# Optimization experiments

Hardware: AMD Instinct MI355X
Metric: run time of the kernel (lower is better)

## Reference

```python
import jax, jax.numpy as jnp
import numpy as np

D, H, DFF, NE, ND, B = 512, 8, 2048, 64, 64, 16

def _ln(x, g, b):
    m = x.mean(-1, keepdims=True)
    v = ((x - m) ** 2).mean(-1, keepdims=True)
    return (x - m) * jax.lax.rsqrt(v + 1e-5) * g + b

def _mha(q, k, v, Wi, bi, Wo, bo, h=H):
    # q,k,v: (L, B, d) seq-first, like torch nn.MultiheadAttention (eval mode)
    Lq, Bb, d = q.shape
    hd = d // h
    Wq, Wk, Wv = jnp.split(Wi, 3, axis=0)
    bq, bk, bv = jnp.split(bi, 3)
    def proj(x, W, bb):
        y = x @ W.T + bb                                  # (L, B, d)
        return y.reshape(x.shape[0], Bb, h, hd).transpose(1, 2, 0, 3)  # (B, h, L, hd)
    qh = proj(q, Wq, bq) * (hd ** -0.5)
    kh = proj(k, Wk, bk)
    vh = proj(v, Wv, bv)
    a = jax.nn.softmax(jnp.einsum('bhqe,bhke->bhqk', qh, kh), axis=-1)
    o = jnp.einsum('bhqk,bhke->bhqe', a, vh).transpose(2, 0, 1, 3).reshape(Lq, Bb, d)
    return o @ Wo.T + bo

def _ffn(x, W1, b1, W2, b2):
    return jax.nn.relu(x @ W1.T + b1) @ W2.T + b2

def _forward(enc, dec, ec_Wi, ec_bi, ec_Wo, ec_bo, dc_Wi, dc_bi, dc_Wo, dc_bo,
             es_Wi, es_bi, es_Wo, es_bo, ds_Wi, ds_bi, ds_Wo, ds_bo,
             eff_W1, eff_b1, eff_W2, eff_b2, dff_W1, dff_b1, dff_W2, dff_b2,
             n_ec_g, n_ec_b, n_es_g, n_es_b, n_ef_g, n_ef_b, n_dc_g, n_dc_b,
             n_dci_g, n_dci_b, n_ds_g, n_ds_b, n_df_g, n_df_b, pW, pWb, pv, pb):
    f_n = _ln(enc, n_ec_g, n_ec_b)   # (ne, B, d) -- normed once, reused for all j
    G_n = _ln(dec, n_dc_g, n_dc_b)   # (nd, B, d)
    # dec_cross for all j at once (key/value is the single token f_j)
    dc_out = jax.vmap(lambda fj: _mha(G_n, fj[None], fj[None], dc_Wi, dc_bi, dc_Wo, dc_bo))(f_n)  # (ne, nd, B, d)
    G_fj = dec[None] + dc_out                            # (ne, nd, B, d)
    G_im = _ln(G_fj, n_dci_g, n_dci_b)
    # enc_cross for all j at once (query is the single token f_j)
    ec_out = jax.vmap(lambda fj, Gj: _mha(fj[None], Gj, Gj, ec_Wi, ec_bi, ec_Wo, ec_bo)[0])(f_n, G_im)  # (ne, B, d)
    enc1 = enc + ec_out
    # attention pooling over the ne fusion copies
    G_c = G_fj.transpose(2, 1, 0, 3)                     # (B, nd, ne, d)
    energy = jnp.tanh(G_c @ pW.T + pWb + pb)
    w = jax.nn.softmax(energy @ pv.T, axis=2)            # (B, nd, ne, 1)
    dec1 = (G_c * w).sum(axis=2).transpose(1, 0, 2)      # (nd, B, d)
    # self-attention + FFN (pre-norm residual)
    en = _ln(enc1, n_es_g, n_es_b)
    enc2 = enc1 + _mha(en, en, en, es_Wi, es_bi, es_Wo, es_bo)
    dn = _ln(dec1, n_ds_g, n_ds_b)
    dec2 = dec1 + _mha(dn, dn, dn, ds_Wi, ds_bi, ds_Wo, ds_bo)
    enc3 = enc2 + _ffn(_ln(enc2, n_ef_g, n_ef_b), eff_W1, eff_b1, eff_W2, eff_b2)
    dec3 = dec2 + _ffn(_ln(dec2, n_df_g, n_df_b), dff_W1, dff_b1, dff_W2, dff_b2)
    return (enc3, dec3)

def setup_inputs() -> dict:
    key = jax.random.key(0)
    ks = iter(jax.random.split(key, 64))
    def w(shape, scale=0.05):
        return jax.random.normal(next(ks), shape, jnp.float32) * scale
    d, dff = D, DFF
    inp = {
        'enc': jax.random.normal(next(ks), (NE, B, d), jnp.float32),
        'dec': jax.random.normal(next(ks), (ND, B, d), jnp.float32),
    }
    for p in ['ec', 'dc', 'es', 'ds']:
        inp[p + '_Wi'] = w((3 * d, d)); inp[p + '_bi'] = jnp.zeros(3 * d, jnp.float32)
        inp[p + '_Wo'] = w((d, d)); inp[p + '_bo'] = jnp.zeros(d, jnp.float32)
    for p in ['eff', 'dff']:
        inp[p + '_W1'] = w((dff, d)); inp[p + '_b1'] = jnp.zeros(dff, jnp.float32)
        inp[p + '_W2'] = w((d, dff)); inp[p + '_b2'] = jnp.zeros(d, jnp.float32)
    for p in ['n_ec', 'n_es', 'n_ef', 'n_dc', 'n_dci', 'n_ds', 'n_df']:
        inp[p + '_g'] = jnp.ones(d, jnp.float32); inp[p + '_b'] = jnp.zeros(d, jnp.float32)
    inp['pW'] = w((d, d)); inp['pWb'] = jnp.zeros(d, jnp.float32)
    inp['pv'] = w((1, d)); inp['pb'] = jnp.zeros(d, jnp.float32)
    return inp

def reference(enc, dec, ec_Wi, ec_bi, ec_Wo, ec_bo, dc_Wi, dc_bi, dc_Wo, dc_bo,
              es_Wi, es_bi, es_Wo, es_bo, ds_Wi, ds_bi, ds_Wo, ds_bo,
              eff_W1, eff_b1, eff_W2, eff_b2, dff_W1, dff_b1, dff_W2, dff_b2,
              n_ec_g, n_ec_b, n_es_g, n_es_b, n_ef_g, n_ef_b, n_dc_g, n_dc_b,
              n_dci_g, n_dci_b, n_ds_g, n_ds_b, n_df_g, n_df_b, pW, pWb, pv, pb):
    return _forward(enc, dec, ec_Wi, ec_bi, ec_Wo, ec_bo, dc_Wi, dc_bi, dc_Wo, dc_bo,
                    es_Wi, es_bi, es_Wo, es_bo, ds_Wi, ds_bi, ds_Wo, ds_bo,
                    eff_W1, eff_b1, eff_W2, eff_b2, dff_W1, dff_b1, dff_W2, dff_b2,
                    n_ec_g, n_ec_b, n_es_g, n_es_b, n_ef_g, n_ef_b, n_dc_g, n_dc_b,
                    n_dci_g, n_dci_b, n_ds_g, n_ds_b, n_df_g, n_df_b, pW, pWb, pv, pb)
```

## Files before the change

kernel.cpp:

```cpp
#include <hip/hip_runtime.h>


typedef __bf16 bf16_t;
typedef bf16_t bf16x8 __attribute__((ext_vector_type(8)));
typedef float f32x4 __attribute__((ext_vector_type(4)));
typedef unsigned short u16x4 __attribute__((ext_vector_type(4)));
typedef unsigned short u16x8 __attribute__((ext_vector_type(8)));

__device__ inline unsigned short f2bf(float f) {
  unsigned int u = __float_as_uint(f);
  u += 0x7fffu + ((u >> 16) & 1u);
  return (unsigned short)(u >> 16);
}
__device__ inline float bf2f(unsigned short u) {
  return __uint_as_float(((unsigned int)u) << 16);
}

__device__ inline float wsum(float v) {
#pragma unroll
  for (int o = 1; o < 64; o <<= 1) v += __shfl_xor(v, o);
  return v;
}
__device__ inline float wmax(float v) {
#pragma unroll
  for (int o = 1; o < 64; o <<= 1) v = fmaxf(v, __shfl_xor(v, o));
  return v;
}

struct CastJob {
  const float* src;
  unsigned short* dst;
  int n;
  const float* cs;
};

__device__ inline void ln_body(const float* __restrict__ x,
                               const float* __restrict__ g,
                               const float* __restrict__ be,
                               unsigned short* __restrict__ y, int t) {
  float v0 = x[t], v1 = x[t + 256];
  float s = wsum(v0 + v1);
  float s2 = wsum(v0 * v0 + v1 * v1);
  __shared__ float sh[8];
  int w = t >> 6, lane = t & 63;
  if (lane == 0) { sh[w] = s; sh[4 + w] = s2; }
  __syncthreads();
  s = sh[0] + sh[1] + sh[2] + sh[3];
  s2 = sh[4] + sh[5] + sh[6] + sh[7];
  float mean = s * (1.f / 512.f);
  float var = s2 * (1.f / 512.f) - mean * mean;
  float r = rsqrtf(var + 1e-5f);
  y[t] = f2bf((v0 - mean) * r * g[t] + be[t]);
  y[t + 256] = f2bf((v1 - mean) * r * g[t + 256] + be[t + 256]);
}

__device__ inline void stats_body(const float* __restrict__ x,
                                  float* __restrict__ m, float* __restrict__ q2,
                                  unsigned short* __restrict__ xb, int t,
                                  int row) {
  float v0 = x[t], v1 = x[t + 256];
  if (xb) {
    xb[t] = f2bf(v0);
    xb[t + 256] = f2bf(v1);
  }
  float s = wsum(v0 + v1);
  float s2 = wsum(v0 * v0 + v1 * v1);
  __shared__ float sh2[8];
  int w = t >> 6, lane = t & 63;
  if (lane == 0) { sh2[w] = s; sh2[4 + w] = s2; }
  __syncthreads();
  if (t == 0) {
    s = sh2[0] + sh2[1] + sh2[2] + sh2[3];
    s2 = sh2[4] + sh2[5] + sh2[6] + sh2[7];
    m[row] = s * (1.f / 512.f);
    q2[row] = s2 * (1.f / 512.f);
  }
}

struct Phase0Args {
  const float* enc; const float* g_ec; const float* b_ec; unsigned short* f_n;
  const float* dec; float* md; float* q2d; unsigned short* dec_b;
  CastJob cast[6];
  const float* Wk; const float* Wv; const float* bk; const float* bv;
  const float* g_dci; const float* b_dci;
  float* u_k; float* u_v; float* c_k; float* c_v;
  float* zbase; int zcount;
};

__global__ __launch_bounds__(256) void phase0(Phase0Args a) {
  int bx = blockIdx.x;
  const int t = threadIdx.x;
  if (bx < 2048) {
    int row = bx;
    if (row < 1024) {
      ln_body(a.enc + (size_t)row * 512, a.g_ec, a.b_ec,
              a.f_n + (size_t)row * 512, t);
    } else {
      row -= 1024;
      stats_body(a.dec + (size_t)row * 512, a.md, a.q2d,
                 a.dec_b + (size_t)row * 512, t, row);
    }
    return;
  }
  bx -= 2048;
  if (bx < 256) {
    const int total = 6 * 262144;
    const int stride = 256 * 256 * 4;
    for (int e = (bx * 256 + t) * 4; e < total; e += stride) {
      int jj = e >> 18;
      int i = e & 262143;
      const CastJob cj = a.cast[jj];
      float4 v = *(const float4*)(cj.src + i);
      if (cj.cs) {
        int k = i & 511;
        v.x *= cj.cs[k]; v.y *= cj.cs[k + 1];
        v.z *= cj.cs[k + 2]; v.w *= cj.cs[k + 3];
      }
      u16x4 o = {f2bf(v.x), f2bf(v.y), f2bf(v.z), f2bf(v.w)};
      *(u16x4*)(cj.dst + i) = o;
    }
    return;
  }
  bx -= 256;
  if (bx < 128) {
    int n = bx * 4 + (t >> 6);
    int lane = t & 63;
    const float* wk = a.Wk + (size_t)n * 512;
    const float* wv = a.Wv + (size_t)n * 512;
    float uk = 0.f, uv = 0.f, ck = 0.f, cv = 0.f;
#pragma unroll
    for (int k0 = 0; k0 < 512; k0 += 64) {
      int k = k0 + lane;
      float x = wk[k], y = wv[k], gg = a.g_dci[k], bb = a.b_dci[k];
      uk += x * gg; ck += x * bb;
      uv += y * gg; cv += y * bb;
    }
    uk = wsum(uk); uv = wsum(uv); ck = wsum(ck); cv = wsum(cv);
    if (lane == 0) {
      a.u_k[n] = uk; a.u_v[n] = uv;
      a.c_k[n] = ck + a.bk[n]; a.c_v[n] = cv + a.bv[n];
    }
    return;
  }
  for (int i = t; i < a.zcount; i += 256) a.zbase[i] = 0.f;
}

struct GemmJob {
  const unsigned short* X;
  const float* Xf;
  const float* Asum; const float* Asq;
  const float* g; const float* be;
  const unsigned short* W;
  const float* bias;
  const float* resid;
  float* Y;
  unsigned short* Ybf;
  float* Ssum; float* Ssq;
  float scale;
  int relu;
};
struct MrJob {
  const unsigned short* A; const unsigned short* B;
  const float* md; const float* q2d;
  const float* ts; const float* tsq;
  float* mArr; float* rArr;
};
struct GemmBatch {
  GemmJob j[5];
  MrJob mr;
  CastJob c[9];
};

__device__ inline u16x8 fold_pack(float4 va, float4 vb, const float* gp,
                                  const float* bp, float m, float ri) {
  float4 g0 = *(const float4*)gp;
  float4 g1 = *(const float4*)(gp + 4);
  float4 e0 = *(const float4*)bp;
  float4 e1 = *(const float4*)(bp + 4);
  u16x8 o;
  o[0] = f2bf((va.x - m) * ri * g0.x + e0.x);
  o[1] = f2bf((va.y - m) * ri * g0.y + e0.y);
  o[2] = f2bf((va.z - m) * ri * g0.z + e0.z);
  o[3] = f2bf((va.w - m) * ri * g0.w + e0.w);
  o[4] = f2bf((vb.x - m) * ri * g1.x + e1.x);
  o[5] = f2bf((vb.y - m) * ri * g1.y + e1.y);
  o[6] = f2bf((vb.z - m) * ri * g1.z + e1.z);
  o[7] = f2bf((vb.w - m) * ri * g1.w + e1.w);
  return o;
}

__global__ __launch_bounds__(256) void gemm_bf16(GemmBatch gb, int M, int N,
                                                 int K, int cast_z, int mr_z) {
  const int t = threadIdx.x;
  if ((int)blockIdx.z == cast_z) {
    const int nb = gridDim.x * gridDim.y;
    const int bid = blockIdx.y * gridDim.x + blockIdx.x;
    const int stride = nb * 256 * 4;
#pragma unroll 1
    for (int jj = 0; jj < 9; ++jj) {
      const CastJob cj = gb.c[jj];
      if (!cj.src) continue;
      for (int i = (bid * 256 + t) * 4; i < cj.n; i += stride) {
        float4 v = *(const float4*)(cj.src + i);
        u16x4 o = {f2bf(v.x), f2bf(v.y), f2bf(v.z), f2bf(v.w)};
        *(u16x4*)(cj.dst + i) = o;
      }
    }
    return;
  }
  __shared__ unsigned short As[64][72];
  __shared__ unsigned short Bs[64][72];
  const int lane = t & 63;
  const int wave = t >> 6;
  const int wr = wave >> 1;
  const int wc = wave & 1;
  const int fr = lane & 15;
  const int fg = lane >> 4;
  const int c1 = t + 256;
  const int r0 = t >> 3, o0 = (t & 7) * 8;
  const int r1 = c1 >> 3, o1 = (c1 & 7) * 8;

  if ((int)blockIdx.z == mr_z) {
    const int bb = blockIdx.y * gridDim.x + blockIdx.x;
    if (bb >= 16) return;
    const unsigned short* Ap = gb.mr.A + (size_t)bb * 512;
    const unsigned short* Bp = gb.mr.B + (size_t)bb * 512;
    f32x4 acc[2][2] = {};
    for (int k0 = 0; k0 < 512; k0 += 64) {
      *(u16x8*)&As[r0][o0] = *(const u16x8*)&Ap[(size_t)r0 * 8192 + k0 + o0];
      *(u16x8*)&As[r1][o1] = *(const u16x8*)&Ap[(size_t)r1 * 8192 + k0 + o1];
      *(u16x8*)&Bs[r0][o0] = *(const u16x8*)&Bp[(size_t)r0 * 8192 + k0 + o0];
      *(u16x8*)&Bs[r1][o1] = *(const u16x8*)&Bp[(size_t)r1 * 8192 + k0 + o1];
      __syncthreads();
#pragma unroll
      for (int ks = 0; ks < 2; ++ks) {
        int kk = ks * 32 + fg * 8;
        bf16x8 a0 = *(const bf16x8*)&As[wr * 32 + fr][kk];
        bf16x8 a1 = *(const bf16x8*)&As[wr * 32 + 16 + fr][kk];
        bf16x8 b0 = *(const bf16x8*)&Bs[wc * 32 + fr][kk];
        bf16x8 b1 = *(const bf16x8*)&Bs[wc * 32 + 16 + fr][kk];
        acc[0][0] = __builtin_amdgcn_mfma_f32_16x16x32_bf16(a0, b0, acc[0][0], 0, 0, 0);
        acc[0][1] = __builtin_amdgcn_mfma_f32_16x16x32_bf16(a0, b1, acc[0][1], 0, 0, 0);
        acc[1][0] = __builtin_amdgcn_mfma_f32_16x16x32_bf16(a1, b0, acc[1][0], 0, 0, 0);
        acc[1][1] = __builtin_amdgcn_mfma_f32_16x16x32_bf16(a1, b1, acc[1][1], 0, 0, 0);
      }
      __syncthreads();
    }
#pragma unroll
    for (int nt = 0; nt < 2; ++nt) {
      int j = wc * 32 + nt * 16 + fr;
      float mtv = gb.mr.ts[j * 16 + bb] * (1.f / 512.f);
      float qtv = gb.mr.tsq[j * 16 + bb] * (1.f / 512.f);
#pragma unroll
      for (int mt = 0; mt < 2; ++mt) {
        int ibase = wr * 32 + mt * 16 + fg * 4;
#pragma unroll
        for (int r = 0; r < 4; ++r) {
          int i = ibase + r;
          float s = acc[mt][nt][r];
          float mean = gb.mr.md[i * 16 + bb] + mtv;
          float msq = gb.mr.q2d[i * 16 + bb] + qtv + s * (2.f / 512.f);
          int idx = bb * 4096 + j * 64 + i;
          gb.mr.mArr[idx] = mean;
          gb.mr.rArr[idx] = rsqrtf(msq - mean * mean + 1e-5f);
        }
      }
    }
    return;
  }

  const GemmJob jb = gb.j[blockIdx.z];
  const int bm = blockIdx.y * 64;
  const int bn = blockIdx.x * 64;
  const bool fold = jb.Xf != nullptr;
  f32x4 acc[2][2] = {};
  const unsigned short* Wp = jb.W + (size_t)bn * K;
  const unsigned short* Xp = jb.X ? jb.X + (size_t)bm * K : nullptr;

  float lm0 = 0.f, lr0i = 0.f, lm1 = 0.f, lr1i = 0.f;
  if (fold) {
    float s = jb.Asum[bm + r0], q = jb.Asq[bm + r0];
    lm0 = s * (1.f / 512.f);
    lr0i = rsqrtf(q * (1.f / 512.f) - lm0 * lm0 + 1e-5f);
    s = jb.Asum[bm + r1]; q = jb.Asq[bm + r1];
    lm1 = s * (1.f / 512.f);
    lr1i = rsqrtf(q * (1.f / 512.f) - lm1 * lm1 + 1e-5f);
  }

  u16x8 xa0, xa1;
  float4 fa0a, fa0b, fa1a, fa1b;
  if (fold) {
    const float* p0 = jb.Xf + (size_t)(bm + r0) * K + o0;
    const float* p1 = jb.Xf + (size_t)(bm + r1) * K + o1;
    fa0a = *(const float4*)p0; fa0b = *(const float4*)(p0 + 4);
    fa1a = *(const float4*)p1; fa1b = *(const float4*)(p1 + 4);
  } else {
    xa0 = *(const u16x8*)&Xp[(size_t)r0 * K + o0];
    xa1 = *(const u16x8*)&Xp[(size_t)r1 * K + o1];
  }
  u16x8 wa0 = *(const u16x8*)&Wp[(size_t)r0 * K + o0];
  u16x8 wa1 = *(const u16x8*)&Wp[(size_t)r1 * K + o1];

  for (int k0 = 0; k0 < K; k0 += 64) {
    if (fold) {
      *(u16x8*)&As[r0][o0] = fold_pack(fa0a, fa0b, jb.g + k0 + o0, jb.be + k0 + o0, lm0, lr0i);
      *(u16x8*)&As[r1][o1] = fold_pack(fa1a, fa1b, jb.g + k0 + o1, jb.be + k0 + o1, lm1, lr1i);
    } else {
      *(u16x8*)&As[r0][o0] = xa0;
      *(u16x8*)&As[r1][o1] = xa1;
    }
    *(u16x8*)&Bs[r0][o0] = wa0;
    *(u16x8*)&Bs[r1][o1] = wa1;
    __syncthreads();
    if (k0 + 64 < K) {
      const int kn = k0 + 64;
      if (fold) {
        const float* p0 = jb.Xf + (size_t)(bm + r0) * K + kn + o0;
        const float* p1 = jb.Xf + (size_t)(bm + r1) * K + kn + o1;
        fa0a = *(const float4*)p0; fa0b = *(const float4*)(p0 + 4);
        fa1a = *(const float4*)p1; fa1b = *(const float4*)(p1 + 4);
      } else {
        xa0 = *(const u16x8*)&Xp[(size_t)r0 * K + kn + o0];
        xa1 = *(const u16x8*)&Xp[(size_t)r1 * K + kn + o1];
      }
      wa0 = *(const u16x8*)&Wp[(size_t)r0 * K + kn + o0];
      wa1 = *(const u16x8*)&Wp[(size_t)r1 * K + kn + o1];
    }
#pragma unroll
    for (int ks = 0; ks < 2; ++ks) {
      int kk = ks * 32 + fg * 8;
      bf16x8 a0 = *(const bf16x8*)&As[wr * 32 + fr][kk];
      bf16x8 a1 = *(const bf16x8*)&As[wr * 32 + 16 + fr][kk];
      bf16x8 b0 = *(const bf16x8*)&Bs[wc * 32 + fr][kk];
      bf16x8 b1 = *(const bf16x8*)&Bs[wc * 32 + 16 + fr][kk];
      acc[0][0] = __builtin_amdgcn_mfma_f32_16x16x32_bf16(a0, b0, acc[0][0], 0, 0, 0);
      acc[0][1] = __builtin_amdgcn_mfma_f32_16x16x32_bf16(a0, b1, acc[0][1], 0, 0, 0);
      acc[1][0] = __builtin_amdgcn_mfma_f32_16x16x32_bf16(a1, b0, acc[1][0], 0, 0, 0);
      acc[1][1] = __builtin_amdgcn_mfma_f32_16x16x32_bf16(a1, b1, acc[1][1], 0, 0, 0);
    }
    __syncthreads();
  }
  float rsum[2][4], rsq[2][4];
  const bool dostat = jb.Ssum != nullptr;
  if (dostat) {
#pragma unroll
    for (int mt = 0; mt < 2; ++mt)
#pragma unroll
      for (int r = 0; r < 4; ++r) { rsum[mt][r] = 0.f; rsq[mt][r] = 0.f; }
  }
#pragma unroll
  for (int mt = 0; mt < 2; ++mt) {
#pragma unroll
    for (int nt = 0; nt < 2; ++nt) {
      int col = bn + wc * 32 + nt * 16 + fr;
      int rowb = bm + wr * 32 + mt * 16 + fg * 4;
      float bia = jb.bias ? jb.bias[col] : 0.f;
#pragma unroll
      for (int r = 0; r < 4; ++r) {
        float v = (acc[mt][nt][r] + bia) * jb.scale;
        if (jb.relu) v = fmaxf(v, 0.f);
        if (jb.resid) v += jb.resid[(size_t)(rowb + r) * N + col];
        size_t idx = (size_t)(rowb + r) * N + col;
        if (jb.Y) jb.Y[idx] = v;
        if (jb.Ybf) jb.Ybf[idx] = f2bf(v);
        if (dostat) { rsum[mt][r] += v; rsq[mt][r] += v * v; }
      }
    }
  }
  if (dostat) {
#pragma unroll
    for (int mt = 0; mt < 2; ++mt)
#pragma unroll
      for (int r = 0; r < 4; ++r) {
        float s = rsum[mt][r], q = rsq[mt][r];
#pragma unroll
        for (int o = 1; o < 16; o <<= 1) {
          s += __shfl_xor(s, o);
          q += __shfl_xor(q, o);
        }
        if (fr == 0) {
          int row = bm + wr * 32 + mt * 16 + fg * 4 + r;
          atomicAdd(&jb.Ssum[row], s);
          atomicAdd(&jb.Ssq[row], q);
        }
      }
  }
}

__global__ __launch_bounds__(256) void attnpool(
    const unsigned short* __restrict__ Qe, const unsigned short* __restrict__ Kd,
    const unsigned short* __restrict__ Kt, const unsigned short* __restrict__ Vd,
    const unsigned short* __restrict__ Vt, const float* __restrict__ u_k,
    const float* __restrict__ u_v, const float* __restrict__ c_k,
    const float* __restrict__ c_v, const float* __restrict__ mArr,
    const float* __restrict__ rArr, unsigned short* __restrict__ O,
    const float* __restrict__ Ed, const float* __restrict__ Et,
    const float* __restrict__ pv, const float* __restrict__ dec,
    const unsigned short* __restrict__ tbf, float* __restrict__ dec1,
    float* __restrict__ d1s, float* __restrict__ d1q) {
  __shared__ unsigned short Qs[64][72];
  __shared__ unsigned short Ks[64][72];
  __shared__ unsigned short VdT[64][72];
  __shared__ unsigned short Ps[64][72];
  __shared__ float ms[64][66];
  __shared__ float rs[64][66];
  __shared__ float stp[64][4], sup[64][4], scp[64][4];
  __shared__ float stv[64], suv[64], scv[64], swv[64], swmv[64];
  __shared__ float esh[64], wsh[64], pps[8];
  const int t = threadIdx.x;
  if (blockIdx.x < 128) {
    int h = blockIdx.x & 7;
    int b = blockIdx.x >> 3;
    {
      int row = t >> 2;
      int qt = t & 3;
      int cb = qt * 16;
      size_t base = (size_t)(row * 16 + b) * 512 + h * 64 + cb;
      u16x8 q0 = *(const u16x8*)(Qe + base);
      u16x8 q1 = *(const u16x8*)(Qe + base + 8);
      u16x8 k0 = *(const u16x8*)(Kd + base);
      u16x8 k1 = *(const u16x8*)(Kd + base + 8);
      u16x8 kt0 = *(const u16x8*)(Kt + base);
      u16x8 kt1 = *(const u16x8*)(Kt + base + 8);
      u16x8 v0 = *(const u16x8*)(Vd + base);
      u16x8 v1 = *(const u16x8*)(Vd + base + 8);
      *(u16x8*)&Qs[row][cb] = q0;
      *(u16x8*)&Qs[row][cb + 8] = q1;
      *(u16x8*)&Ks[row][cb] = k0;
      *(u16x8*)&Ks[row][cb + 8] = k1;
#pragma unroll
      for (int jj = 0; jj < 8; ++jj) VdT[cb + jj][row] = v0[jj];
#pragma unroll
      for (int jj = 0; jj < 8; ++jj) VdT[cb + 8 + jj][row] = v1[jj];
      float st_ = 0.f, su_ = 0.f, sc_ = 0.f;
#pragma unroll
      for (int jj = 0; jj < 8; ++jj) {
        float qa = bf2f(q0[jj]), qb = bf2f(q1[jj]);
        st_ += qa * bf2f(kt0[jj]) + qb * bf2f(kt1[jj]);
        su_ += qa * u_k[h * 64 + cb + jj] + qb * u_k[h * 64 + cb + 8 + jj];
        sc_ += qa * c_k[h * 64 + cb + jj] + qb * c_k[h * 64 + cb + 8 + jj];
      }
      stp[row][qt] = st_;
      sup[row][qt] = su_;
      scp[row][qt] = sc_;
    }
#pragma unroll
    for (int k = 0; k < 16; ++k) {
      int idx = t + k * 256;
      ms[idx >> 6][idx & 63] = mArr[(size_t)b * 4096 + idx];
      rs[idx >> 6][idx & 63] = rArr[(size_t)b * 4096 + idx];
    }
    __syncthreads();
    if (t < 64) {
      stv[t] = stp[t][0] + stp[t][1] + stp[t][2] + stp[t][3];
      suv[t] = sup[t][0] + sup[t][1] + sup[t][2] + sup[t][3];
      scv[t] = scp[t][0] + scp[t][1] + scp[t][2] + scp[t][3];
    }
    __syncthreads();
    int wave = t >> 6, lane = t & 63;
    int fr = lane & 15, fg = lane >> 4;
    f32x4 sacc[4] = {};
    bf16x8 aq0 = *(const bf16x8*)&Qs[wave * 16 + fr][fg * 8];
    bf16x8 aq1 = *(const bf16x8*)&Qs[wave * 16 + fr][32 + fg * 8];
#pragma unroll
    for (int nt = 0; nt < 4; ++nt) {
      bf16x8 b0 = *(const bf16x8*)&Ks[nt * 16 + fr][fg * 8];
      bf16x8 b1 = *(const bf16x8*)&Ks[nt * 16 + fr][32 + fg * 8];
      sacc[nt] = __builtin_amdgcn_mfma_f32_16x16x32_bf16(aq0, b0, sacc[nt], 0, 0, 0);
      sacc[nt] = __builtin_amdgcn_mfma_f32_16x16x32_bf16(aq1, b1, sacc[nt], 0, 0, 0);
    }
#pragma unroll
    for (int r = 0; r < 4; ++r) {
      int j = wave * 16 + fg * 4 + r;
      float stj = stv[j], suj = suv[j], scj = scv[j];
      float a0, a1, a2, a3;
      {
        int i0 = fr, i1 = 16 + fr, i2 = 32 + fr, i3 = 48 + fr;
        a0 = rs[j][i0] * (sacc[0][r] + stj - ms[j][i0] * suj) + scj;
        a1 = rs[j][i1] * (sacc[1][r] + stj - ms[j][i1] * suj) + scj;
        a2 = rs[j][i2] * (sacc[2][r] + stj - ms[j][i2] * suj) + scj;
        a3 = rs[j][i3] * (sacc[3][r] + stj - ms[j][i3] * suj) + scj;
      }
      float mx = fmaxf(fmaxf(a0, a1), fmaxf(a2, a3));
#pragma unroll
      for (int o = 1; o < 16; o <<= 1) mx = fmaxf(mx, __shfl_xor(mx, o));
      a0 = __expf(a0 - mx);
      a1 = __expf(a1 - mx);
      a2 = __expf(a2 - mx);
      a3 = __expf(a3 - mx);
      float se = a0 + a1 + a2 + a3;
#pragma unroll
      for (int o = 1; o < 16; o <<= 1) se += __shfl_xor(se, o);
      float inv = 1.f / se;
      float w0 = a0 * inv * rs[j][fr];
      float w1 = a1 * inv * rs[j][16 + fr];
      float w2 = a2 * inv * rs[j][32 + fr];
      float w3 = a3 * inv * rs[j][48 + fr];
      float sw = w0 + w1 + w2 + w3;
      float swm = w0 * ms[j][fr] + w1 * ms[j][16 + fr] + w2 * ms[j][32 + fr] +
                  w3 * ms[j][48 + fr];
#pragma unroll
      for (int o = 1; o < 16; o <<= 1) {
        sw += __shfl_xor(sw, o);
        swm += __shfl_xor(swm, o);
      }
      Ps[j][fr] = f2bf(w0);
      Ps[j][16 + fr] = f2bf(w1);
      Ps[j][32 + fr] = f2bf(w2);
      Ps[j][48 + fr] = f2bf(w3);
      if (fr == 0) {
        swv[j] = sw;
        swmv[j] = swm;
      }
    }
    f32x4 oc[4] = {};
    bf16x8 ap0 = *(const bf16x8*)&Ps[wave * 16 + fr][fg * 8];
    bf16x8 ap1 = *(const bf16x8*)&Ps[wave * 16 + fr][32 + fg * 8];
#pragma unroll
    for (int nt = 0; nt < 4; ++nt) {
      bf16x8 b0 = *(const bf16x8*)&VdT[nt * 16 + fr][fg * 8];
      bf16x8 b1 = *(const bf16x8*)&VdT[nt * 16 + fr][32 + fg * 8];
      oc[nt] = __builtin_amdgcn_mfma_f32_16x16x32_bf16(ap0, b0, oc[nt], 0, 0, 0);
      oc[nt] = __builtin_amdgcn_mfma_f32_16x16x32_bf16(ap1, b1, oc[nt], 0, 0, 0);
    }
#pragma unroll
    for (int nt = 0; nt < 4; ++nt) {
      int d = nt * 16 + fr;
      float uvd = u_v[h * 64 + d];
      float cvd = c_v[h * 64 + d];
#pragma unroll
      for (int r = 0; r < 4; ++r) {
        int j = wave * 16 + fg * 4 + r;
        size_t gidx = (size_t)(j * 16 + b) * 512 + h * 64 + d;
        float o = oc[nt][r] + swv[j] * bf2f(Vt[gidx]) - swmv[j] * uvd + cvd;
        O[gidx] = f2bf(o);
      }
    }
    return;
  }
  int idx = blockIdx.x - 128;
  int i = idx & 63;
  int b = idx >> 6;
  int wave = t >> 6, lane = t & 63;
  float edv[8], pvv[8];
  const float* ed = Ed + (size_t)(i * 16 + b) * 512;
#pragma unroll
  for (int c = 0; c < 8; ++c) {
    edv[c] = ed[c * 64 + lane];
    pvv[c] = pv[c * 64 + lane];
  }
#pragma unroll 1
  for (int jl = 0; jl < 16; ++jl) {
    int j = wave * 16 + jl;
    const float* et = Et + (size_t)(j * 16 + b) * 512;
    float s = 0.f;
#pragma unroll
    for (int c = 0; c < 8; ++c) {
      float x = edv[c] + et[c * 64 + lane];
      float e2 = __expf(2.f * x);
      float th = 1.f - 2.f * __builtin_amdgcn_rcpf(e2 + 1.f);
      s += th * pvv[c];
    }
    s = wsum(s);
    if (lane == 0) esh[j] = s;
  }
  __syncthreads();
  if (t < 64) {
    float e = esh[t];
    float mx = wmax(e);
    float ex = __expf(e - mx);
    float se = wsum(ex);
    wsh[t] = ex / se;
  }
  __syncthreads();
  size_t rowib = (size_t)(i * 16 + b) * 512;
  int d2 = t * 2;
  float2 dv = *(const float2*)(dec + rowib + d2);
  float acc0 = dv.x, acc1 = dv.y;
#pragma unroll 8
  for (int j2 = 0; j2 < 64; ++j2) {
    const unsigned short* tp = tbf + (size_t)(j2 * 16 + b) * 512 + d2;
    float w = wsh[j2];
    acc0 += w * bf2f(tp[0]);
    acc1 += w * bf2f(tp[1]);
  }
  float2 ov = {acc0, acc1};
  *(float2*)(dec1 + rowib + d2) = ov;
  float s1 = acc0 + acc1;
  float s2v = acc0 * acc0 + acc1 * acc1;
  s1 = wsum(s1);
  s2v = wsum(s2v);
  if (lane == 0) { pps[wave] = s1; pps[4 + wave] = s2v; }
  __syncthreads();
  if (t == 0) {
    d1s[i * 16 + b] = pps[0] + pps[1] + pps[2] + pps[3];
    d1q[i * 16 + b] = pps[4] + pps[5] + pps[6] + pps[7];
  }
}

__global__ __launch_bounds__(256) void self_attn(
    const unsigned short* __restrict__ QKVe, unsigned short* __restrict__ Oe,
    const unsigned short* __restrict__ QKVd, unsigned short* __restrict__ Od) {
  const unsigned short* QKV = blockIdx.y ? QKVd : QKVe;
  unsigned short* O = blockIdx.y ? Od : Oe;
  int h = blockIdx.x & 7;
  int b = blockIdx.x >> 3;
  __shared__ unsigned short Qs[64][72];
  __shared__ unsigned short Ksh[64][72];
  __shared__ unsigned short VT[64][72];
  __shared__ unsigned short Ps[64][72];
  int t = threadIdx.x;
  {
    int row = t >> 2;
    int cb = (t & 3) * 16;
    const unsigned short* src =
        QKV + (size_t)(row * 16 + b) * 1536 + h * 64 + cb;
    u16x8 q0 = *(const u16x8*)(src);
    u16x8 q1 = *(const u16x8*)(src + 8);
    u16x8 k0 = *(const u16x8*)(src + 512);
    u16x8 k1 = *(const u16x8*)(src + 520);
    u16x8 v0 = *(const u16x8*)(src + 1024);
    u16x8 v1 = *(const u16x8*)(src + 1032);
    *(u16x8*)&Qs[row][cb] = q0;
    *(u16x8*)&Qs[row][cb + 8] = q1;
    *(u16x8*)&Ksh[row][cb] = k0;
    *(u16x8*)&Ksh[row][cb + 8] = k1;
#pragma unroll
    for (int jj = 0; jj < 8; ++jj) VT[cb + jj][row] = v0[jj];
#pragma unroll
    for (int jj = 0; jj < 8; ++jj) VT[cb + 8 + jj][row] = v1[jj];
  }
  __syncthreads();
  int wave = t >> 6, lane = t & 63;
  int fr = lane & 15, fg = lane >> 4;
  f32x4 sc[4] = {};
  bf16x8 aq0 = *(const bf16x8*)&Qs[wave * 16 + fr][fg * 8];
  bf16x8 aq1 = *(const bf16x8*)&Qs[wave * 16 + fr][32 + fg * 8];
#pragma unroll
  for (int nt = 0; nt < 4; ++nt) {
    bf16x8 b0 = *(const bf16x8*)&Ksh[nt * 16 + fr][fg * 8];
    bf16x8 b1 = *(const bf16x8*)&Ksh[nt * 16 + fr][32 + fg * 8];
    sc[nt] = __builtin_amdgcn_mfma_f32_16x16x32_bf16(aq0, b0, sc[nt], 0, 0, 0);
    sc[nt] = __builtin_amdgcn_mfma_f32_16x16x32_bf16(aq1, b1, sc[nt], 0, 0, 0);
  }
#pragma unroll
  for (int r = 0; r < 4; ++r) {
    float a0 = sc[0][r] * 0.125f, a1 = sc[1][r] * 0.125f;
    float a2 = sc[2][r] * 0.125f, a3 = sc[3][r] * 0.125f;
    float mx = fmaxf(fmaxf(a0, a1), fmaxf(a2, a3));
#pragma unroll
    for (int o = 1; o < 16; o <<= 1) mx = fmaxf(mx, __shfl_xor(mx, o));
    a0 = __expf(a0 - mx);
    a1 = __expf(a1 - mx);
    a2 = __expf(a2 - mx);
    a3 = __expf(a3 - mx);
    float se = a0 + a1 + a2 + a3;
#pragma unroll
    for (int o = 1; o < 16; o <<= 1) se += __shfl_xor(se, o);
    float inv = 1.f / se;
    int prow = wave * 16 + fg * 4 + r;
    Ps[prow][0 + fr] = f2bf(a0 * inv);
    Ps[prow][16 + fr] = f2bf(a1 * inv);
    Ps[prow][32 + fr] = f2bf(a2 * inv);
    Ps[prow][48 + fr] = f2bf(a3 * inv);
  }
  f32x4 oc[4] = {};
  bf16x8 ap0 = *(const bf16x8*)&Ps[wave * 16 + fr][fg * 8];
  bf16x8 ap1 = *(const bf16x8*)&Ps[wave * 16 + fr][32 + fg * 8];
#pragma unroll
  for (int nt = 0; nt < 4; ++nt) {
    bf16x8 b0 = *(const bf16x8*)&VT[nt * 16 + fr][fg * 8];
    bf16x8 b1 = *(const bf16x8*)&VT[nt * 16 + fr][32 + fg * 8];
    oc[nt] = __builtin_amdgcn_mfma_f32_16x16x32_bf16(ap0, b0, oc[nt], 0, 0, 0);
    oc[nt] = __builtin_amdgcn_mfma_f32_16x16x32_bf16(ap1, b1, oc[nt], 0, 0, 0);
  }
#pragma unroll
  for (int nt = 0; nt < 4; ++nt) {
#pragma unroll
    for (int r = 0; r < 4; ++r) {
      int q = wave * 16 + fg * 4 + r;
      int d = nt * 16 + fr;
      O[(size_t)(q * 16 + b) * 512 + h * 64 + d] = f2bf(oc[nt][r]);
    }
  }
}

extern "C" void kernel_launch(void* const* d_in, const int* in_sizes, int n_in,
                              void* d_out, int out_size, void* d_ws,
                              size_t ws_size, hipStream_t stream) {
  const float* enc = (const float*)d_in[0];
  const float* dec = (const float*)d_in[1];
  const float* ec_Wi = (const float*)d_in[2];
  const float* ec_bi = (const float*)d_in[3];
  const float* ec_Wo = (const float*)d_in[4];
  const float* ec_bo = (const float*)d_in[5];
  const float* dc_Wi = (const float*)d_in[6];
  const float* dc_bi = (const float*)d_in[7];
  const float* dc_Wo = (const float*)d_in[8];
  const float* dc_bo = (const float*)d_in[9];
  const float* es_Wi = (const float*)d_in[10];
  const float* es_bi = (const float*)d_in[11];
  const float* es_Wo = (const float*)d_in[12];
  const float* es_bo = (const float*)d_in[13];
  const float* ds_Wi = (const float*)d_in[14];
  const float* ds_bi = (const float*)d_in[15];
  const float* ds_Wo = (const float*)d_in[16];
  const float* ds_bo = (const float*)d_in[17];
  const float* eff_W1 = (const float*)d_in[18];
  const float* eff_b1 = (const float*)d_in[19];
  const float* eff_W2 = (const float*)d_in[20];
  const float* eff_b2 = (const float*)d_in[21];
  const float* dff_W1 = (const float*)d_in[22];
  const float* dff_b1 = (const float*)d_in[23];
  const float* dff_W2 = (const float*)d_in[24];
  const float* dff_b2 = (const float*)d_in[25];
  const float* n_ec_g = (const float*)d_in[26];
  const float* n_ec_b = (const float*)d_in[27];
  const float* n_es_g = (const float*)d_in[28];
  const float* n_es_b = (const float*)d_in[29];
  const float* n_ef_g = (const float*)d_in[30];
  const float* n_ef_b = (const float*)d_in[31];
  const float* n_dci_g = (const float*)d_in[34];
  const float* n_dci_b = (const float*)d_in[35];
  const float* n_ds_g = (const float*)d_in[36];
  const float* n_ds_b = (const float*)d_in[37];
  const float* n_df_g = (const float*)d_in[38];
  const float* n_df_b = (const float*)d_in[39];
  const float* pW = (const float*)d_in[40];
  const float* pWb = (const float*)d_in[41];
  const float* pv = (const float*)d_in[42];
  const float* pb = (const float*)d_in[43];

  float* ws = (float*)d_ws;
  const size_t U = 524288;
  float* Ed = ws + 3 * U;
  float* Et = ws + 7 * U;
  float* enc1 = ws + 8 * U;
  float* dec1 = ws + 9 * U;
  float* enc2 = ws + 10 * U;
  float* dec2 = ws + 11 * U;
  float* sm = ws + 12 * U;
  float* md = sm;
  float* q2d = sm + 1024;
  float* u_k = sm + 4096;
  float* u_v = sm + 4608;
  float* c_k = sm + 5120;
  float* c_v = sm + 5632;
  float* mArr = sm + 6144;
  float* rArr = sm + 6144 + 65536;
  float* stx = ws + 24 * U;
  float* t_s = stx;
  float* t_sq = stx + 1024;
  float* e1s = stx + 2048;
  float* e1q = stx + 3072;
  float* d1s = stx + 4096;
  float* d1q = stx + 5120;
  float* e2s = stx + 6144;
  float* e2q = stx + 7168;
  float* d2s = stx + 8192;
  float* d2q = stx + 9216;
  unsigned short* ub0 = (unsigned short*)ws;
  unsigned short* Qe_b = ub0 + 0 * U;
  unsigned short* Kd_b = ub0 + 1 * U;
  unsigned short* Vd_b = ub0 + 2 * U;
  unsigned short* Kt_b = ub0 + 3 * U;
  unsigned short* Vt_b = ub0 + 4 * U;
  unsigned short* ub = (unsigned short*)(ws + 12 * U + 137216);
  const int W262 = 262144, W786 = 786432, W1M = 1048576;
  unsigned short* w_dcWv = ub;
  unsigned short* w_ecWq = w_dcWv + W262;
  unsigned short* w_ecWkg = w_ecWq + W262;
  unsigned short* w_ecWvg = w_ecWkg + W262;
  unsigned short* w_pW = w_ecWvg + W262;
  unsigned short* w_dcWo = w_pW + W262;
  unsigned short* w_ecWo = w_dcWo + W262;
  unsigned short* w_esWi = w_ecWo + W262;
  unsigned short* w_dsWi = w_esWi + W786;
  unsigned short* w_esWo = w_dsWi + W786;
  unsigned short* w_dsWo = w_esWo + W262;
  unsigned short* w_effW1 = w_dsWo + W262;
  unsigned short* w_dffW1 = w_effW1 + W1M;
  unsigned short* w_effW2 = w_dffW1 + W1M;
  unsigned short* w_dffW2 = w_effW2 + W1M;
  unsigned short* actb = w_dffW2 + W1M;
  unsigned short* f_n_b = actb;
  unsigned short* V1_b = actb + U;
  unsigned short* dec_b = actb + 2 * U;
  unsigned short* tb_b = actb + 3 * U;
  unsigned short* Oec_b = actb + 4 * U;
  unsigned short* OaE = dec_b;
  unsigned short* OaD = tb_b;
  unsigned short* QKVe_b = (unsigned short*)(ws + 0 * U);
  unsigned short* QKVd_b = (unsigned short*)(ws + 2 * U);
  unsigned short* He_b = (unsigned short*)(ws + 0 * U);
  unsigned short* Hd_b = (unsigned short*)(ws + 2 * U);

  const float* dc_Wv = dc_Wi + 1024 * 512;
  const float* dc_bv = dc_bi + 1024;
  const float* ec_Wq = ec_Wi;
  const float* ec_bq = ec_bi;
  const float* ec_Wk = ec_Wi + 512 * 512;
  const float* ec_bk = ec_bi + 512;
  const float* ec_Wv = ec_Wi + 1024 * 512;
  const float* ec_bv = ec_bi + 1024;

  auto J = [](const unsigned short* X, const unsigned short* W,
              const float* bias, const float* resid, float* Y,
              unsigned short* Ybf, float scale, int relu) {
    GemmJob j{};
    j.X = X; j.W = W; j.bias = bias; j.resid = resid;
    j.Y = Y; j.Ybf = Ybf; j.scale = scale; j.relu = relu;
    return j;
  };
  auto JF = [](const float* Xf, const float* As, const float* Aq,
               const float* g, const float* be, const unsigned short* W,
               const float* bias, unsigned short* Ybf, int relu) {
    GemmJob j{};
    j.Xf = Xf; j.Asum = As; j.Asq = Aq; j.g = g; j.be = be;
    j.W = W; j.bias = bias; j.Ybf = Ybf; j.scale = 1.f; j.relu = relu;
    return j;
  };

  {
    Phase0Args pa{};
    pa.enc = enc; pa.g_ec = n_ec_g; pa.b_ec = n_ec_b; pa.f_n = f_n_b;
    pa.dec = dec; pa.md = md; pa.q2d = q2d; pa.dec_b = dec_b;
    pa.cast[0] = {dc_Wv, w_dcWv, W262, nullptr};
    pa.cast[1] = {ec_Wq, w_ecWq, W262, nullptr};
    pa.cast[2] = {ec_Wk, w_ecWkg, W262, n_dci_g};
    pa.cast[3] = {ec_Wv, w_ecWvg, W262, n_dci_g};
    pa.cast[4] = {pW, w_pW, W262, nullptr};
    pa.cast[5] = {dc_Wo, w_dcWo, W262, nullptr};
    pa.Wk = ec_Wk; pa.Wv = ec_Wv; pa.bk = ec_bk; pa.bv = ec_bv;
    pa.g_dci = n_dci_g; pa.b_dci = n_dci_b;
    pa.u_k = u_k; pa.u_v = u_v; pa.c_k = c_k; pa.c_v = c_v;
    pa.zbase = stx; pa.zcount = 10240;
    phase0<<<2433, 256, 0, stream>>>(pa);
  }
  {
    GemmBatch gb{};
    gb.j[0] = J(f_n_b, w_dcWv, dc_bv, nullptr, nullptr, V1_b, 1.f, 0);
    gb.j[1] = J(f_n_b, w_ecWq, ec_bq, nullptr, nullptr, Qe_b, 0.125f, 0);
    gb.j[2] = J(dec_b, w_ecWkg, nullptr, nullptr, nullptr, Kd_b, 1.f, 0);
    gb.j[3] = J(dec_b, w_ecWvg, nullptr, nullptr, nullptr, Vd_b, 1.f, 0);
    gb.j[4] = J(dec_b, w_pW, pWb, nullptr, Ed, nullptr, 1.f, 0);
    gb.c[0] = {ec_Wo, w_ecWo, W262, nullptr};
    gb.c[1] = {es_Wi, w_esWi, W786, nullptr};
    gb.c[2] = {ds_Wi, w_dsWi, W786, nullptr};
    gb.c[3] = {es_Wo, w_esWo, W262, nullptr};
    gb.c[4] = {ds_Wo, w_dsWo, W262, nullptr};
    gb.c[5] = {eff_W1, w_effW1, W1M, nullptr};
    gb.c[6] = {dff_W1, w_dffW1, W1M, nullptr};
    gb.c[7] = {eff_W2, w_effW2, W1M, nullptr};
    gb.c[8] = {dff_W2, w_dffW2, W1M, nullptr};
    gemm_bf16<<<dim3(8, 16, 6), 256, 0, stream>>>(gb, 1024, 512, 512, 5, -1);
  }
  {
    GemmBatch gb{};
    gb.j[0] = J(V1_b, w_dcWo, dc_bo, nullptr, nullptr, tb_b, 1.f, 0);
    gb.j[0].Ssum = t_s; gb.j[0].Ssq = t_sq;
    gemm_bf16<<<dim3(8, 16, 1), 256, 0, stream>>>(gb, 1024, 512, 512, -1, -1);
  }
  {
    GemmBatch gb{};
    gb.j[0] = J(tb_b, w_ecWkg, nullptr, nullptr, nullptr, Kt_b, 1.f, 0);
    gb.j[1] = J(tb_b, w_ecWvg, nullptr, nullptr, nullptr, Vt_b, 1.f, 0);
    gb.j[2] = J(tb_b, w_pW, pb, nullptr, Et, nullptr, 1.f, 0);
    gb.mr = {dec_b, tb_b, md, q2d, t_s, t_sq, mArr, rArr};
    gemm_bf16<<<dim3(8, 16, 4), 256, 0, stream>>>(gb, 1024, 512, 512, -1, 3);
  }
  attnpool<<<1152, 256, 0, stream>>>(Qe_b, Kd_b, Kt_b, Vd_b, Vt_b, u_k, u_v,
                                     c_k, c_v, mArr, rArr, Oec_b, Ed, Et, pv,
                                     dec, tb_b, dec1, d1s, d1q);
  {
    GemmBatch gb{};
    gb.j[0] = J(Oec_b, w_ecWo, ec_bo, enc, enc1, nullptr, 1.f, 0);
    gb.j[0].Ssum = e1s; gb.j[0].Ssq = e1q;
    gemm_bf16<<<dim3(8, 16, 1), 256, 0, stream>>>(gb, 1024, 512, 512, -1, -1);
  }
  {
    GemmBatch gb{};
    gb.j[0] = JF(enc1, e1s, e1q, n_es_g, n_es_b, w_esWi, es_bi, QKVe_b, 0);
    gb.j[1] = JF(dec1, d1s, d1q, n_ds_g, n_ds_b, w_dsWi, ds_bi, QKVd_b, 0);
    gemm_bf16<<<dim3(24, 16, 2), 256, 0, stream>>>(gb, 1024, 1536, 512, -1, -1);
  }
  self_attn<<<dim3(128, 2), 256, 0, stream>>>(QKVe_b, OaE, QKVd_b, OaD);
  {
    GemmBatch gb{};
    gb.j[0] = J(OaE, w_esWo, es_bo, enc1, enc2, nullptr, 1.f, 0);
    gb.j[0].Ssum = e2s; gb.j[0].Ssq = e2q;
    gb.j[1] = J(OaD, w_dsWo, ds_bo, dec1, dec2, nullptr, 1.f, 0);
    gb.j[1].Ssum = d2s; gb.j[1].Ssq = d2q;
    gemm_bf16<<<dim3(8, 16, 2), 256, 0, stream>>>(gb, 1024, 512, 512, -1, -1);
  }
  {
    GemmBatch gb{};
    gb.j[0] = JF(enc2, e2s, e2q, n_ef_g, n_ef_b, w_effW1, eff_b1, He_b, 1);
    gb.j[1] = JF(dec2, d2s, d2q, n_df_g, n_df_b, w_dffW1, dff_b1, Hd_b, 1);
    gemm_bf16<<<dim3(32, 16, 2), 256, 0, stream>>>(gb, 1024, 2048, 512, -1, -1);
  }
  float* out = (float*)d_out;
  {
    GemmBatch gb{};
    gb.j[0] = J(He_b, w_effW2, eff_b2, enc2, out, nullptr, 1.f, 0);
    gb.j[1] = J(Hd_b, w_dffW2, dff_b2, dec2, out + U, nullptr, 1.f, 0);
    gemm_bf16<<<dim3(8, 16, 2), 256, 0, stream>>>(gb, 1024, 512, 2048, -1, -1);
  }
}
```

Baseline: 339.8 us.

## Move attention pooling into ec_Wo GEMM launch and template GEMM variants

The attention-pooling work moves out of the combined attnpool kernel and into extra z-slices of the following ec_Wo GEMM launch, so ec_attn now runs alone with 128 blocks and pooling overlaps the GEMM. The GEMM kernel is templated on its extra-work mode, LayerNorm folding and stats epilogue, which turns runtime branches into compile-time ones. Pooling now competes with the GEMM for the same launch and shares its LDS footprint, which may lower occupancy for the pooling blocks.

```diff
diff --git a/kernel.cpp b/kernel.cpp
--- a/kernel.cpp
+++ b/kernel.cpp
@@ -165,10 +165,15 @@
   const float* ts; const float* tsq;
   float* mArr; float* rArr;
 };
+struct PoolJob {
+  const float* Ed; const float* Et; const float* pv; const float* dec;
+  const unsigned short* tbf; float* dec1; float* d1s; float* d1q;
+};
 struct GemmBatch {
   GemmJob j[5];
   MrJob mr;
   CastJob c[9];
+  PoolJob pl;
 };
 
 __device__ inline u16x8 fold_pack(float4 va, float4 vb, const float* gp,
@@ -189,24 +194,95 @@
   return o;
 }
 
+__device__ void pool_body(const PoolJob& p, int i, int b) {
+  __shared__ float esh[64], wsh[64], pps[8];
+  const int t = threadIdx.x;
+  int wave = t >> 6, lane = t & 63;
+  float edv[8], pvv[8];
+  const float* ed = p.Ed + (size_t)(i * 16 + b) * 512;
+#pragma unroll
+  for (int c = 0; c < 8; ++c) {
+    edv[c] = ed[c * 64 + lane];
+    pvv[c] = p.pv[c * 64 + lane];
+  }
+#pragma unroll 1
+  for (int jl = 0; jl < 16; ++jl) {
+    int j = wave * 16 + jl;
+    const float* et = p.Et + (size_t)(j * 16 + b) * 512;
+    float s = 0.f;
+#pragma unroll
+    for (int c = 0; c < 8; ++c) {
+      float x = edv[c] + et[c * 64 + lane];
+      float e2 = __expf(2.f * x);
+      float th = 1.f - 2.f * __builtin_amdgcn_rcpf(e2 + 1.f);
+      s += th * pvv[c];
+    }
+    s = wsum(s);
+    if (lane == 0) esh[j] = s;
+  }
+  __syncthreads();
+  if (t < 64) {
+    float e = esh[t];
+    float mx = wmax(e);
+    float ex = __expf(e - mx);
+    float se = wsum(ex);
+    wsh[t] = ex / se;
+  }
+  __syncthreads();
+  size_t rowib = (size_t)(i * 16 + b) * 512;
+  int d2 = t * 2;
+  float2 dv = *(const float2*)(p.dec + rowib + d2);
+  float acc0 = dv.x, acc1 = dv.y;
+#pragma unroll 8
+  for (int j2 = 0; j2 < 64; ++j2) {
+    const unsigned short* tp = p.tbf + (size_t)(j2 * 16 + b) * 512 + d2;
+    float w = wsh[j2];
+    acc0 += w * bf2f(tp[0]);
+    acc1 += w * bf2f(tp[1]);
+  }
+  float2 ov = {acc0, acc1};
+  *(float2*)(p.dec1 + rowib + d2) = ov;
+  float s1 = acc0 + acc1;
+  float s2v = acc0 * acc0 + acc1 * acc1;
+  s1 = wsum(s1);
+  s2v = wsum(s2v);
+  if (lane == 0) { pps[wave] = s1; pps[4 + wave] = s2v; }
+  __syncthreads();
+  if (t == 0) {
+    p.d1s[i * 16 + b] = pps[0] + pps[1] + pps[2] + pps[3];
+    p.d1q[i * 16 + b] = pps[4] + pps[5] + pps[6] + pps[7];
+  }
+}
+
+template <int EXTRA, bool FOLD, bool STATS>
 __global__ __launch_bounds__(256) void gemm_bf16(GemmBatch gb, int M, int N,
-                                                 int K, int cast_z, int mr_z) {
+                                                 int K, int xz) {
   const int t = threadIdx.x;
-  if ((int)blockIdx.z == cast_z) {
-    const int nb = gridDim.x * gridDim.y;
-    const int bid = blockIdx.y * gridDim.x + blockIdx.x;
-    const int stride = nb * 256 * 4;
+  if constexpr (EXTRA == 1) {
+    if ((int)blockIdx.z == xz) {
+      const int nb = gridDim.x * gridDim.y;
+      const int bid = blockIdx.y * gridDim.x + blockIdx.x;
+      const int stride = nb * 256 * 4;
 #pragma unroll 1
-    for (int jj = 0; jj < 9; ++jj) {
-      const CastJob cj = gb.c[jj];
-      if (!cj.src) continue;
-      for (int i = (bid * 256 + t) * 4; i < cj.n; i += stride) {
-        float4 v = *(const float4*)(cj.src + i);
-        u16x4 o = {f2bf(v.x), f2bf(v.y), f2bf(v.z), f2bf(v.w)};
-        *(u16x4*)(cj.dst + i) = o;
+      for (int jj = 0; jj < 9; ++jj) {
+        const CastJob cj = gb.c[jj];
+        if (!cj.src) continue;
+        for (int i = (bid * 256 + t) * 4; i < cj.n; i += stride) {
+          float4 v = *(const float4*)(cj.src + i);
+          u16x4 o = {f2bf(v.x), f2bf(v.y), f2bf(v.z), f2bf(v.w)};
+          *(u16x4*)(cj.dst + i) = o;
+        }
       }
-    }
-    return;
+      return;
+    }
+  }
+  if constexpr (EXTRA == 3) {
+    if ((int)blockIdx.z >= xz) {
+      int pb = ((int)blockIdx.z - xz) * (int)(gridDim.x * gridDim.y) +
+               (int)blockIdx.y * (int)gridDim.x + (int)blockIdx.x;
+      pool_body(gb.pl, pb & 63, pb >> 6);
+      return;
+    }
   }
   __shared__ unsigned short As[64][72];
   __shared__ unsigned short Bs[64][72];
@@ -220,81 +296,80 @@
   const int r0 = t >> 3, o0 = (t & 7) * 8;
   const int r1 = c1 >> 3, o1 = (c1 & 7) * 8;
 
-  if ((int)blockIdx.z == mr_z) {
-    const int bb = blockIdx.y * gridDim.x + blockIdx.x;
-    if (bb >= 16) return;
-    const unsigned short* Ap = gb.mr.A + (size_t)bb * 512;
-    const unsigned short* Bp = gb.mr.B + (size_t)bb * 512;
-    f32x4 acc[2][2] = {};
-    for (int k0 = 0; k0 < 512; k0 += 64) {
-      *(u16x8*)&As[r0][o0] = *(const u16x8*)&Ap[(size_t)r0 * 8192 + k0 + o0];
-      *(u16x8*)&As[r1][o1] = *(const u16x8*)&Ap[(size_t)r1 * 8192 + k0 + o1];
-      *(u16x8*)&Bs[r0][o0] = *(const u16x8*)&Bp[(size_t)r0 * 8192 + k0 + o0];
-      *(u16x8*)&Bs[r1][o1] = *(const u16x8*)&Bp[(size_t)r1 * 8192 + k0 + o1];
-      __syncthreads();
-#pragma unroll
-      for (int ks = 0; ks < 2; ++ks) {
-        int kk = ks * 32 + fg * 8;
-        bf16x8 a0 = *(const bf16x8*)&As[wr * 32 + fr][kk];
-        bf16x8 a1 = *(const bf16x8*)&As[wr * 32 + 16 + fr][kk];
-        bf16x8 b0 = *(const bf16x8*)&Bs[wc * 32 + fr][kk];
-        bf16x8 b1 = *(const bf16x8*)&Bs[wc * 32 + 16 + fr][kk];
-        acc[0][0] = __builtin_amdgcn_mfma_f32_16x16x32_bf16(a0, b0, acc[0][0], 0, 0, 0);
-        acc[0][1] = __builtin_amdgcn_mfma_f32_16x16x32_bf16(a0, b1, acc[0][1], 0, 0, 0);
-        acc[1][0] = __builtin_amdgcn_mfma_f32_16x16x32_bf16(a1, b0, acc[1][0], 0, 0, 0);
-        acc[1][1] = __builtin_amdgcn_mfma_f32_16x16x32_bf16(a1, b1, acc[1][1], 0, 0, 0);
+  if constexpr (EXTRA == 2) {
+    if ((int)blockIdx.z == xz) {
+      const int bb = blockIdx.y * gridDim.x + blockIdx.x;
+      if (bb >= 16) return;
+      const unsigned short* Ap = gb.mr.A + (size_t)bb * 512;
+      const unsigned short* Bp = gb.mr.B + (size_t)bb * 512;
+      f32x4 acc[2][2] = {};
+      for (int k0 = 0; k0 < 512; k0 += 64) {
+        *(u16x8*)&As[r0][o0] = *(const u16x8*)&Ap[(size_t)r0 * 8192 + k0 + o0];
+        *(u16x8*)&As[r1][o1] = *(const u16x8*)&Ap[(size_t)r1 * 8192 + k0 + o1];
+        *(u16x8*)&Bs[r0][o0] = *(const u16x8*)&Bp[(size_t)r0 * 8192 + k0 + o0];
+        *(u16x8*)&Bs[r1][o1] = *(const u16x8*)&Bp[(size_t)r1 * 8192 + k0 + o1];
+        __syncthreads();
+#pragma unroll
+        for (int ks = 0; ks < 2; ++ks) {
+          int kk = ks * 32 + fg * 8;
+          bf16x8 a0 = *(const bf16x8*)&As[wr * 32 + fr][kk];
+          bf16x8 a1 = *(const bf16x8*)&As[wr * 32 + 16 + fr][kk];
+          bf16x8 b0 = *(const bf16x8*)&Bs[wc * 32 + fr][kk];
+          bf16x8 b1 = *(const bf16x8*)&Bs[wc * 32 + 16 + fr][kk];
+          acc[0][0] = __builtin_amdgcn_mfma_f32_16x16x32_bf16(a0, b0, acc[0][0], 0, 0, 0);
+          acc[0][1] = __builtin_amdgcn_mfma_f32_16x16x32_bf16(a0, b1, acc[0][1], 0, 0, 0);
+          acc[1][0] = __builtin_amdgcn_mfma_f32_16x16x32_bf16(a1, b0, acc[1][0], 0, 0, 0);
+          acc[1][1] = __builtin_amdgcn_mfma_f32_16x16x32_bf16(a1, b1, acc[1][1], 0, 0, 0);
+        }
+        __syncthreads();
       }
-      __syncthreads();
-    }
-#pragma unroll
-    for (int nt = 0; nt < 2; ++nt) {
-      int j = wc * 32 + nt * 16 + fr;
-      float mtv = gb.mr.ts[j * 16 + bb] * (1.f / 512.f);
-      float qtv = gb.mr.tsq[j * 16 + bb] * (1.f / 512.f);
-#pragma unroll
-      for (int mt = 0; mt < 2; ++mt) {
-        int ibase = wr * 32 + mt * 16 + fg * 4;
-#pragma unroll
-        for (int r = 0; r < 4; ++r) {
-          int i = ibase + r;
-          float s = acc[mt][nt][r];
-          float mean = gb.mr.md[i * 16 + bb] + mtv;
-          float msq = gb.mr.q2d[i * 16 + bb] + qtv + s * (2.f / 512.f);
-          int idx = bb * 4096 + j * 64 + i;
-          gb.mr.mArr[idx] = mean;
-          gb.mr.rArr[idx] = rsqrtf(msq - mean * mean + 1e-5f);
+#pragma unroll
+      for (int nt = 0; nt < 2; ++nt) {
+        int j = wc * 32 + nt * 16 + fr;
+        float mtv = gb.mr.ts[j * 16 + bb] * (1.f / 512.f);
+        float qtv = gb.mr.tsq[j * 16 + bb] * (1.f / 512.f);
+#pragma unroll
+        for (int mt = 0; mt < 2; ++mt) {
+          int ibase = wr * 32 + mt * 16 + fg * 4;
+#pragma unroll
+          for (int r = 0; r < 4; ++r) {
+            int i = ibase + r;
+            float s = acc[mt][nt][r];
+            float mean = gb.mr.md[i * 16 + bb] + mtv;
+            float msq = gb.mr.q2d[i * 16 + bb] + qtv + s * (2.f / 512.f);
+            int idx = bb * 4096 + j * 64 + i;
+            gb.mr.mArr[idx] = mean;
+            gb.mr.rArr[idx] = rsqrtf(msq - mean * mean + 1e-5f);
+          }
         }
       }
-    }
-    return;
+      return;
+    }
   }
 
   const GemmJob jb = gb.j[blockIdx.z];
   const int bm = blockIdx.y * 64;
   const int bn = blockIdx.x * 64;
-  const bool fold = jb.Xf != nullptr;
   f32x4 acc[2][2] = {};
   const unsigned short* Wp = jb.W + (size_t)bn * K;
-  const unsigned short* Xp = jb.X ? jb.X + (size_t)bm * K : nullptr;
-
+
+  u16x8 xa0, xa1;
+  float4 fa0a, fa0b, fa1a, fa1b;
   float lm0 = 0.f, lr0i = 0.f, lm1 = 0.f, lr1i = 0.f;
-  if (fold) {
+  const unsigned short* Xp = nullptr;
+  if constexpr (FOLD) {
     float s = jb.Asum[bm + r0], q = jb.Asq[bm + r0];
     lm0 = s * (1.f / 512.f);
     lr0i = rsqrtf(q * (1.f / 512.f) - lm0 * lm0 + 1e-5f);
     s = jb.Asum[bm + r1]; q = jb.Asq[bm + r1];
     lm1 = s * (1.f / 512.f);
     lr1i = rsqrtf(q * (1.f / 512.f) - lm1 * lm1 + 1e-5f);
-  }
-
-  u16x8 xa0, xa1;
-  float4 fa0a, fa0b, fa1a, fa1b;
-  if (fold) {
     const float* p0 = jb.Xf + (size_t)(bm + r0) * K + o0;
     const float* p1 = jb.Xf + (size_t)(bm + r1) * K + o1;
     fa0a = *(const float4*)p0; fa0b = *(const float4*)(p0 + 4);
     fa1a = *(const float4*)p1; fa1b = *(const float4*)(p1 + 4);
   } else {
+    Xp = jb.X + (size_t)bm * K;
     xa0 = *(const u16x8*)&Xp[(size_t)r0 * K + o0];
     xa1 = *(const u16x8*)&Xp[(size_t)r1 * K + o1];
   }
@@ -302,7 +377,7 @@
   u16x8 wa1 = *(const u16x8*)&Wp[(size_t)r1 * K + o1];
 
   for (int k0 = 0; k0 < K; k0 += 64) {
-    if (fold) {
+    if constexpr (FOLD) {
       *(u16x8*)&As[r0][o0] = fold_pack(fa0a, fa0b, jb.g + k0 + o0, jb.be + k0 + o0, lm0, lr0i);
       *(u16x8*)&As[r1][o1] = fold_pack(fa1a, fa1b, jb.g + k0 + o1, jb.be + k0 + o1, lm1, lr1i);
     } else {
@@ -314,7 +389,7 @@
     __syncthreads();
     if (k0 + 64 < K) {
       const int kn = k0 + 64;
-      if (fold) {
+      if constexpr (FOLD) {
         const float* p0 = jb.Xf + (size_t)(bm + r0) * K + kn + o0;
         const float* p1 = jb.Xf + (size_t)(bm + r1) * K + kn + o1;
         fa0a = *(const float4*)p0; fa0b = *(const float4*)(p0 + 4);
@@ -341,8 +416,7 @@
     __syncthreads();
   }
   float rsum[2][4], rsq[2][4];
-  const bool dostat = jb.Ssum != nullptr;
-  if (dostat) {
+  if constexpr (STATS) {
 #pragma unroll
     for (int mt = 0; mt < 2; ++mt)
 #pragma unroll
@@ -363,11 +437,11 @@
         size_t idx = (size_t)(rowb + r) * N + col;
         if (jb.Y) jb.Y[idx] = v;
         if (jb.Ybf) jb.Ybf[idx] = f2bf(v);
-        if (dostat) { rsum[mt][r] += v; rsq[mt][r] += v * v; }
+        if constexpr (STATS) { rsum[mt][r] += v; rsq[mt][r] += v * v; }
       }
     }
   }
-  if (dostat) {
+  if constexpr (STATS) {
 #pragma unroll
     for (int mt = 0; mt < 2; ++mt)
 #pragma unroll
@@ -387,17 +461,15 @@
   }
 }
 
-__global__ __launch_bounds__(256) void attnpool(
+__global__ __launch_bounds__(256) void ec_attn(
     const unsigned short* __restrict__ Qe, const unsigned short* __restrict__ Kd,
     const unsigned short* __restrict__ Kt, const unsigned short* __restrict__ Vd,
     const unsigned short* __restrict__ Vt, const float* __restrict__ u_k,
     const float* __restrict__ u_v, const float* __restrict__ c_k,
     const float* __restrict__ c_v, const float* __restrict__ mArr,
-    const float* __restrict__ rArr, unsigned short* __restrict__ O,
-    const float* __restrict__ Ed, const float* __restrict__ Et,
-    const float* __restrict__ pv, const float* __restrict__ dec,
-    const unsigned short* __restrict__ tbf, float* __restrict__ dec1,
-    float* __restrict__ d1s, float* __restrict__ d1q) {
+    const float* __restrict__ rArr, unsigned short* __restrict__ O) {
+  int h = blockIdx.x & 7;
+  int b = blockIdx.x >> 3;
   __shared__ unsigned short Qs[64][72];
   __shared__ unsigned short Ks[64][72];
   __shared__ unsigned short VdT[64][72];
@@ -406,195 +478,131 @@
   __shared__ float rs[64][66];
   __shared__ float stp[64][4], sup[64][4], scp[64][4];
   __shared__ float stv[64], suv[64], scv[64], swv[64], swmv[64];
-  __shared__ float esh[64], wsh[64], pps[8];
-  const int t = threadIdx.x;
-  if (blockIdx.x < 128) {
-    int h = blockIdx.x & 7;
-    int b = blockIdx.x >> 3;
+  int t = threadIdx.x;
+  {
+    int row = t >> 2;
+    int qt = t & 3;
+    int cb = qt * 16;
+    size_t base = (size_t)(row * 16 + b) * 512 + h * 64 + cb;
+    u16x8 q0 = *(const u16x8*)(Qe + base);
+    u16x8 q1 = *(const u16x8*)(Qe + base + 8);
+    u16x8 k0 = *(const u16x8*)(Kd + base);
+    u16x8 k1 = *(const u16x8*)(Kd + base + 8);
+    u16x8 kt0 = *(const u16x8*)(Kt + base);
+    u16x8 kt1 = *(const u16x8*)(Kt + base + 8);
+    u16x8 v0 = *(const u16x8*)(Vd + base);
+    u16x8 v1 = *(const u16x8*)(Vd + base + 8);
+    *(u16x8*)&Qs[row][cb] = q0;
+    *(u16x8*)&Qs[row][cb + 8] = q1;
+    *(u16x8*)&Ks[row][cb] = k0;
+    *(u16x8*)&Ks[row][cb + 8] = k1;
+#pragma unroll
+    for (int jj = 0; jj < 8; ++jj) VdT[cb + jj][row] = v0[jj];
+#pragma unroll
+    for (int jj = 0; jj < 8; ++jj) VdT[cb + 8 + jj][row] = v1[jj];
+    float st_ = 0.f, su_ = 0.f, sc_ = 0.f;
+#pragma unroll
+    for (int jj = 0; jj < 8; ++jj) {
+      float qa = bf2f(q0[jj]), qb = bf2f(q1[jj]);
+      st_ += qa * bf2f(kt0[jj]) + qb * bf2f(kt1[jj]);
+      su_ += qa * u_k[h * 64 + cb + jj] + qb * u_k[h * 64 + cb + 8 + jj];
+      sc_ += qa * c_k[h * 64 + cb + jj] + qb * c_k[h * 64 + cb + 8 + jj];
+    }
+    stp[row][qt] = st_;
+    sup[row][qt] = su_;
+    scp[row][qt] = sc_;
+  }
+#pragma unroll
+  for (int k = 0; k < 16; ++k) {
+    int idx = t + k * 256;
+    ms[idx >> 6][idx & 63] = mArr[(size_t)b * 4096 + idx];
+    rs[idx >> 6][idx & 63] = rArr[(size_t)b * 4096 + idx];
+  }
+  __syncthreads();
+  if (t < 64) {
+    stv[t] = stp[t][0] + stp[t][1] + stp[t][2] + stp[t][3];
+    suv[t] = sup[t][0] + sup[t][1] + sup[t][2] + sup[t][3];
+    scv[t] = scp[t][0] + scp[t][1] + scp[t][2] + scp[t][3];
+  }
+  __syncthreads();
+  int wave = t >> 6, lane = t & 63;
+  int fr = lane & 15, fg = lane >> 4;
+  f32x4 sacc[4] = {};
+  bf16x8 aq0 = *(const bf16x8*)&Qs[wave * 16 + fr][fg * 8];
+  bf16x8 aq1 = *(const bf16x8*)&Qs[wave * 16 + fr][32 + fg * 8];
+#pragma unroll
+  for (int nt = 0; nt < 4; ++nt) {
+    bf16x8 b0 = *(const bf16x8*)&Ks[nt * 16 + fr][fg * 8];
+    bf16x8 b1 = *(const bf16x8*)&Ks[nt * 16 + fr][32 + fg * 8];
+    sacc[nt] = __builtin_amdgcn_mfma_f32_16x16x32_bf16(aq0, b0, sacc[nt], 0, 0, 0);
+    sacc[nt] = __builtin_amdgcn_mfma_f32_16x16x32_bf16(aq1, b1, sacc[nt], 0, 0, 0);
+  }
+#pragma unroll
+  for (int r = 0; r < 4; ++r) {
+    int j = wave * 16 + fg * 4 + r;
+    float stj = stv[j], suj = suv[j], scj = scv[j];
+    float a0, a1, a2, a3;
     {
-      int row = t >> 2;
-      int qt = t & 3;
-      int cb = qt * 16;
-      size_t base = (size_t)(row * 16 + b) * 512 + h * 64 + cb;
-      u16x8 q0 = *(const u16x8*)(Qe + base);
-      u16x8 q1 = *(const u16x8*)(Qe + base + 8);
-      u16x8 k0 = *(const u16x8*)(Kd + base);
-      u16x8 k1 = *(const u16x8*)(Kd + base + 8);
-      u16x8 kt0 = *(const u16x8*)(Kt + base);
-      u16x8 kt1 = *(const u16x8*)(Kt + base + 8);
-      u16x8 v0 = *(const u16x8*)(Vd + base);
-      u16x8 v1 = *(const u16x8*)(Vd + base + 8);
-      *(u16x8*)&Qs[row][cb] = q0;
-      *(u16x8*)&Qs[row][cb + 8] = q1;
-      *(u16x8*)&Ks[row][cb] = k0;
-      *(u16x8*)&Ks[row][cb + 8] = k1;
-#pragma unroll
-      for (int jj = 0; jj < 8; ++jj) VdT[cb + jj][row] = v0[jj];
-#pragma unroll
-      for (int jj = 0; jj < 8; ++jj) VdT[cb + 8 + jj][row] = v1[jj];
-      float st_ = 0.f, su_ = 0.f, sc_ = 0.f;
-#pragma unroll
-      for (int jj = 0; jj < 8; ++jj) {
-        float qa = bf2f(q0[jj]), qb = bf2f(q1[jj]);
-        st_ += qa * bf2f(kt0[jj]) + qb * bf2f(kt1[jj]);
-        su_ += qa * u_k[h * 64 + cb + jj] + qb * u_k[h * 64 + cb + 8 + jj];
-        sc_ += qa * c_k[h * 64 + cb + jj] + qb * c_k[h * 64 + cb + 8 + jj];
-      }
-      stp[row][qt] = st_;
-      sup[row][qt] = su_;
-      scp[row][qt] = sc_;
-    }
-#pragma unroll
-    for (int k = 0; k < 16; ++k) {
-      int idx = t + k * 256;
-      ms[idx >> 6][idx & 63] = mArr[(size_t)b * 4096 + idx];
-      rs[idx >> 6][idx & 63] = rArr[(size_t)b * 4096 + idx];
-    }
-    __syncthreads();
-    if (t < 64) {
-      stv[t] = stp[t][0] + stp[t][1] + stp[t][2] + stp[t][3];
-      suv[t] = sup[t][0] + sup[t][1] + sup[t][2] + sup[t][3];
-      scv[t] = scp[t][0] + scp[t][1] + scp[t][2] + scp[t][3];
-    }
-    __syncthreads();
-    int wave = t >> 6, lane = t & 63;
-    int fr = lane & 15, fg = lane >> 4;
-    f32x4 sacc[4] = {};
-    bf16x8 aq0 = *(const bf16x8*)&Qs[wave * 16 + fr][fg * 8];
-    bf16x8 aq1 = *(const bf16x8*)&Qs[wave * 16 + fr][32 + fg * 8];
-#pragma unroll
-    for (int nt = 0; nt < 4; ++nt) {
-      bf16x8 b0 = *(const bf16x8*)&Ks[nt * 16 + fr][fg * 8];
-      bf16x8 b1 = *(const bf16x8*)&Ks[nt * 16 + fr][32 + fg * 8];
-      sacc[nt] = __builtin_amdgcn_mfma_f32_16x16x32_bf16(aq0, b0, sacc[nt], 0, 0, 0);
-      sacc[nt] = __builtin_amdgcn_mfma_f32_16x16x32_bf16(aq1, b1, sacc[nt], 0, 0, 0);
-    }
+      int i0 = fr, i1 = 16 + fr, i2 = 32 + fr, i3 = 48 + fr;
+      a0 = rs[j][i0] * (sacc[0][r] + stj - ms[j][i0] * suj) + scj;
+      a1 = rs[j][i1] * (sacc[1][r] + stj - ms[j][i1] * suj) + scj;
+      a2 = rs[j][i2] * (sacc[2][r] + stj - ms[j][i2] * suj) + scj;
+      a3 = rs[j][i3] * (sacc[3][r] + stj - ms[j][i3] * suj) + scj;
+    }
+    float mx = fmaxf(fmaxf(a0, a1), fmaxf(a2, a3));
+#pragma unroll
+    for (int o = 1; o < 16; o <<= 1) mx = fmaxf(mx, __shfl_xor(mx, o));
+    a0 = __expf(a0 - mx);
+    a1 = __expf(a1 - mx);
+    a2 = __expf(a2 - mx);
+    a3 = __expf(a3 - mx);
+    float se = a0 + a1 + a2 + a3;
+#pragma unroll
+    for (int o = 1; o < 16; o <<= 1) se += __shfl_xor(se, o);
+    float inv = 1.f / se;
+    float w0 = a0 * inv * rs[j][fr];
+    float w1 = a1 * inv * rs[j][16 + fr];
+    float w2 = a2 * inv * rs[j][32 + fr];
+    float w3 = a3 * inv * rs[j][48 + fr];
+    float sw = w0 + w1 + w2 + w3;
+    float swm = w0 * ms[j][fr] + w1 * ms[j][16 + fr] + w2 * ms[j][32 + fr] +
+                w3 * ms[j][48 + fr];
+#pragma unroll
+    for (int o = 1; o < 16; o <<= 1) {
+      sw += __shfl_xor(sw, o);
+      swm += __shfl_xor(swm, o);
+    }
+    Ps[j][fr] = f2bf(w0);
+    Ps[j][16 + fr] = f2bf(w1);
+    Ps[j][32 + fr] = f2bf(w2);
+    Ps[j][48 + fr] = f2bf(w3);
+    if (fr == 0) {
+      swv[j] = sw;
+      swmv[j] = swm;
+    }
+  }
+  f32x4 oc[4] = {};
+  bf16x8 ap0 = *(const bf16x8*)&Ps[wave * 16 + fr][fg * 8];
+  bf16x8 ap1 = *(const bf16x8*)&Ps[wave * 16 + fr][32 + fg * 8];
+#pragma unroll
+  for (int nt = 0; nt < 4; ++nt) {
+    bf16x8 b0 = *(const bf16x8*)&VdT[nt * 16 + fr][fg * 8];
+    bf16x8 b1 = *(const bf16x8*)&VdT[nt * 16 + fr][32 + fg * 8];
+    oc[nt] = __builtin_amdgcn_mfma_f32_16x16x32_bf16(ap0, b0, oc[nt], 0, 0, 0);
+    oc[nt] = __builtin_amdgcn_mfma_f32_16x16x32_bf16(ap1, b1, oc[nt], 0, 0, 0);
+  }
+#pragma unroll
+  for (int nt = 0; nt < 4; ++nt) {
+    int d = nt * 16 + fr;
+    float uvd = u_v[h * 64 + d];
+    float cvd = c_v[h * 64 + d];
 #pragma unroll
     for (int r = 0; r < 4; ++r) {
       int j = wave * 16 + fg * 4 + r;
-      float stj = stv[j], suj = suv[j], scj = scv[j];
-      float a0, a1, a2, a3;
-      {
-        int i0 = fr, i1 = 16 + fr, i2 = 32 + fr, i3 = 48 + fr;
-        a0 = rs[j][i0] * (sacc[0][r] + stj - ms[j][i0] * suj) + scj;
-        a1 = rs[j][i1] * (sacc[1][r] + stj - ms[j][i1] * suj) + scj;
-        a2 = rs[j][i2] * (sacc[2][r] + stj - ms[j][i2] * suj) + scj;
-        a3 = rs[j][i3] * (sacc[3][r] + stj - ms[j][i3] * suj) + scj;
-      }
-      float mx = fmaxf(fmaxf(a0, a1), fmaxf(a2, a3));
-#pragma unroll
-      for (int o = 1; o < 16; o <<= 1) mx = fmaxf(mx, __shfl_xor(mx, o));
-      a0 = __expf(a0 - mx);
-      a1 = __expf(a1 - mx);
-      a2 = __expf(a2 - mx);
-      a3 = __expf(a3 - mx);
-      float se = a0 + a1 + a2 + a3;
-#pragma unroll
-      for (int o = 1; o < 16; o <<= 1) se += __shfl_xor(se, o);
-      float inv = 1.f / se;
-      float w0 = a0 * inv * rs[j][fr];
-      float w1 = a1 * inv * rs[j][16 + fr];
-      float w2 = a2 * inv * rs[j][32 + fr];
-      float w3 = a3 * inv * rs[j][48 + fr];
-      float sw = w0 + w1 + w2 + w3;
-      float swm = w0 * ms[j][fr] + w1 * ms[j][16 + fr] + w2 * ms[j][32 + fr] +
-                  w3 * ms[j][48 + fr];
-#pragma unroll
-      for (int o = 1; o < 16; o <<= 1) {
-        sw += __shfl_xor(sw, o);
-        swm += __shfl_xor(swm, o);
-      }
-      Ps[j][fr] = f2bf(w0);
-      Ps[j][16 + fr] = f2bf(w1);
-      Ps[j][32 + fr] = f2bf(w2);
-      Ps[j][48 + fr] = f2bf(w3);
-      if (fr == 0) {
-        swv[j] = sw;
-        swmv[j] = swm;
-      }
-    }
-    f32x4 oc[4] = {};
-    bf16x8 ap0 = *(const bf16x8*)&Ps[wave * 16 + fr][fg * 8];
-    bf16x8 ap1 = *(const bf16x8*)&Ps[wave * 16 + fr][32 + fg * 8];
-#pragma unroll
-    for (int nt = 0; nt < 4; ++nt) {
-      bf16x8 b0 = *(const bf16x8*)&VdT[nt * 16 + fr][fg * 8];
-      bf16x8 b1 = *(const bf16x8*)&VdT[nt * 16 + fr][32 + fg * 8];
-      oc[nt] = __builtin_amdgcn_mfma_f32_16x16x32_bf16(ap0, b0, oc[nt], 0, 0, 0);
-      oc[nt] = __builtin_amdgcn_mfma_f32_16x16x32_bf16(ap1, b1, oc[nt], 0, 0, 0);
-    }
-#pragma unroll
-    for (int nt = 0; nt < 4; ++nt) {
-      int d = nt * 16 + fr;
-      float uvd = u_v[h * 64 + d];
-      float cvd = c_v[h * 64 + d];
-#pragma unroll
-      for (int r = 0; r < 4; ++r) {
-        int j = wave * 16 + fg * 4 + r;
-        size_t gidx = (size_t)(j * 16 + b) * 512 + h * 64 + d;
-        float o = oc[nt][r] + swv[j] * bf2f(Vt[gidx]) - swmv[j] * uvd + cvd;
-        O[gidx] = f2bf(o);
-      }
-    }
-    return;
-  }
-  int idx = blockIdx.x - 128;
-  int i = idx & 63;
-  int b = idx >> 6;
-  int wave = t >> 6, lane = t & 63;
-  float edv[8], pvv[8];
-  const float* ed = Ed + (size_t)(i * 16 + b) * 512;
-#pragma unroll
-  for (int c = 0; c < 8; ++c) {
-    edv[c] = ed[c * 64 + lane];
-    pvv[c] = pv[c * 64 + lane];
-  }
-#pragma unroll 1
-  for (int jl = 0; jl < 16; ++jl) {
-    int j = wave * 16 + jl;
-    const float* et = Et + (size_t)(j * 16 + b) * 512;
-    float s = 0.f;
-#pragma unroll
-    for (int c = 0; c < 8; ++c) {
-      float x = edv[c] + et[c * 64 + lane];
-      float e2 = __expf(2.f * x);
-      float th = 1.f - 2.f * __builtin_amdgcn_rcpf(e2 + 1.f);
-      s += th * pvv[c];
-    }
-    s = wsum(s);
-    if (lane == 0) esh[j] = s;
-  }
-  __syncthreads();
-  if (t < 64) {
-    float e = esh[t];
-    float mx = wmax(e);
-    float ex = __expf(e - mx);
-    float se = wsum(ex);
-    wsh[t] = ex / se;
-  }
-  __syncthreads();
-  size_t rowib = (size_t)(i * 16 + b) * 512;
-  int d2 = t * 2;
-  float2 dv = *(const float2*)(dec + rowib + d2);
-  float acc0 = dv.x, acc1 = dv.y;
-#pragma unroll 8
-  for (int j2 = 0; j2 < 64; ++j2) {
-    const unsigned short* tp = tbf + (size_t)(j2 * 16 + b) * 512 + d2;
-    float w = wsh[j2];
-    acc0 += w * bf2f(tp[0]);
-    acc1 += w * bf2f(tp[1]);
-  }
-  float2 ov = {acc0, acc1};
-  *(float2*)(dec1 + rowib + d2) = ov;
-  float s1 = acc0 + acc1;
-  float s2v = acc0 * acc0 + acc1 * acc1;
-  s1 = wsum(s1);
-  s2v = wsum(s2v);
-  if (lane == 0) { pps[wave] = s1; pps[4 + wave] = s2v; }
-  __syncthreads();
-  if (t == 0) {
-    d1s[i * 16 + b] = pps[0] + pps[1] + pps[2] + pps[3];
-    d1q[i * 16 + b] = pps[4] + pps[5] + pps[6] + pps[7];
+      size_t gidx = (size_t)(j * 16 + b) * 512 + h * 64 + d;
+      float o = oc[nt][r] + swv[j] * bf2f(Vt[gidx]) - swmv[j] * uvd + cvd;
+      O[gidx] = f2bf(o);
+    }
   }
 }
 
@@ -853,13 +861,15 @@
     gb.c[6] = {dff_W1, w_dffW1, W1M, nullptr};
     gb.c[7] = {eff_W2, w_effW2, W1M, nullptr};
     gb.c[8] = {dff_W2, w_dffW2, W1M, nullptr};
-    gemm_bf16<<<dim3(8, 16, 6), 256, 0, stream>>>(gb, 1024, 512, 512, 5, -1);
+    gemm_bf16<1, false, false><<<dim3(8, 16, 6), 256, 0, stream>>>(
+        gb, 1024, 512, 512, 5);
   }
   {
     GemmBatch gb{};
     gb.j[0] = J(V1_b, w_dcWo, dc_bo, nullptr, nullptr, tb_b, 1.f, 0);
     gb.j[0].Ssum = t_s; gb.j[0].Ssq = t_sq;
-    gemm_bf16<<<dim3(8, 16, 1), 256, 0, stream>>>(gb, 1024, 512, 512, -1, -1);
+    gemm_bf16<0, false, true><<<dim3(8, 16, 1), 256, 0, stream>>>(
+        gb, 1024, 512, 512, -1);
   }
   {
     GemmBatch gb{};
@@ -867,22 +877,25 @@
     gb.j[1] = J(tb_b, w_ecWvg, nullptr, nullptr, nullptr, Vt_b, 1.f, 0);
     gb.j[2] = J(tb_b, w_pW, pb, nullptr, Et, nullptr, 1.f, 0);
     gb.mr = {dec_b, tb_b, md, q2d, t_s, t_sq, mArr, rArr};
-    gemm_bf16<<<dim3(8, 16, 4), 256, 0, stream>>>(gb, 1024, 512, 512, -1, 3);
-  }
-  attnpool<<<1152, 256, 0, stream>>>(Qe_b, Kd_b, Kt_b, Vd_b, Vt_b, u_k, u_v,
-                                     c_k, c_v, mArr, rArr, Oec_b, Ed, Et, pv,
-                                     dec, tb_b, dec1, d1s, d1q);
+    gemm_bf16<2, false, false><<<dim3(8, 16, 4), 256, 0, stream>>>(
+        gb, 1024, 512, 512, 3);
+  }
+  ec_attn<<<128, 256, 0, stream>>>(Qe_b, Kd_b, Kt_b, Vd_b, Vt_b, u_k, u_v, c_k,
+                                   c_v, mArr, rArr, Oec_b);
   {
     GemmBatch gb{};
     gb.j[0] = J(Oec_b, w_ecWo, ec_bo, enc, enc1, nullptr, 1.f, 0);
     gb.j[0].Ssum = e1s; gb.j[0].Ssq = e1q;
-    gemm_bf16<<<dim3(8, 16, 1), 256, 0, stream>>>(gb, 1024, 512, 512, -1, -1);
+    gb.pl = {Ed, Et, pv, dec, tb_b, dec1, d1s, d1q};
+    gemm_bf16<3, false, true><<<dim3(8, 16, 9), 256, 0, stream>>>(
+        gb, 1024, 512, 512, 1);
   }
   {
     GemmBatch gb{};
     gb.j[0] = JF(enc1, e1s, e1q, n_es_g, n_es_b, w_esWi, es_bi, QKVe_b, 0);
     gb.j[1] = JF(dec1, d1s, d1q, n_ds_g, n_ds_b, w_dsWi, ds_bi, QKVd_b, 0);
-    gemm_bf16<<<dim3(24, 16, 2), 256, 0, stream>>>(gb, 1024, 1536, 512, -1, -1);
+    gemm_bf16<0, true, false><<<dim3(24, 16, 2), 256, 0, stream>>>(
+        gb, 1024, 1536, 512, -1);
   }
   self_attn<<<dim3(128, 2), 256, 0, stream>>>(QKVe_b, OaE, QKVd_b, OaD);
   {
@@ -891,19 +904,22 @@
     gb.j[0].Ssum = e2s; gb.j[0].Ssq = e2q;
     gb.j[1] = J(OaD, w_dsWo, ds_bo, dec1, dec2, nullptr, 1.f, 0);
     gb.j[1].Ssum = d2s; gb.j[1].Ssq = d2q;
-    gemm_bf16<<<dim3(8, 16, 2), 256, 0, stream>>>(gb, 1024, 512, 512, -1, -1);
+    gemm_bf16<0, false, true><<<dim3(8, 16, 2), 256, 0, stream>>>(
+        gb, 1024, 512, 512, -1);
   }
   {
     GemmBatch gb{};
     gb.j[0] = JF(enc2, e2s, e2q, n_ef_g, n_ef_b, w_effW1, eff_b1, He_b, 1);
     gb.j[1] = JF(dec2, d2s, d2q, n_df_g, n_df_b, w_dffW1, dff_b1, Hd_b, 1);
-    gemm_bf16<<<dim3(32, 16, 2), 256, 0, stream>>>(gb, 1024, 2048, 512, -1, -1);
+    gemm_bf16<0, true, false><<<dim3(32, 16, 2), 256, 0, stream>>>(
+        gb, 1024, 2048, 512, -1);
   }
   float* out = (float*)d_out;
   {
     GemmBatch gb{};
     gb.j[0] = J(He_b, w_effW2, eff_b2, enc2, out, nullptr, 1.f, 0);
     gb.j[1] = J(Hd_b, w_dffW2, dff_b2, dec2, out + U, nullptr, 1.f, 0);
-    gemm_bf16<<<dim3(8, 16, 2), 256, 0, stream>>>(gb, 1024, 512, 2048, -1, -1);
-  }
-}
+    gemm_bf16<0, false, false><<<dim3(8, 16, 2), 256, 0, stream>>>(
+        gb, 1024, 512, 2048, -1);
+  }
+}
```

Result: faster. 310.3 us (-8.7%).
